# Kernel tuning notes

Hardware: AMD Instinct MI355X
Metric: run time of the kernel (lower is better)

The kernel has to match this reference:

```python
import jax, jax.numpy as jnp
import numpy as np

N_AGENTS = 8
N_HEADS = 4
HYP = 128   # hypernet_embed
EMB = 32    # mixing_embed_dim


def _hypernet(entities, entity_mask, fc1_w, fc1_b, attn_w, out_w, out_b, fc2_w, fc2_b):
    # entities: [B, ne, ed]; entity_mask: [B, ne] (1 = masked/inactive)
    B, ne, _ = entities.shape
    hd = HYP // N_HEADS
    x1 = jax.nn.relu(entities @ fc1_w + fc1_b)                      # [B, ne, HYP]
    am = entity_mask[:, :N_AGENTS].astype(x1.dtype)                 # [B, na]
    em = entity_mask.astype(x1.dtype)                               # [B, ne]
    # attn_mask[b,i,j] = 1 - (1-am[i])*(1-em[j]): mask if agent i OR entity j inactive
    pre_mask = 1.0 - (1.0 - am)[:, :, None] * (1.0 - em)[:, None, :]  # [B, na, ne]
    # EntityAttentionLayer: agents are the queries, all entities are keys/values
    qkv = x1 @ attn_w                                               # [B, ne, 3*HYP] (no bias)
    q, k, v = jnp.split(qkv, 3, axis=-1)
    q = q[:, :N_AGENTS].reshape(B, N_AGENTS, N_HEADS, hd)
    k = k.reshape(B, ne, N_HEADS, hd)
    v = v.reshape(B, ne, N_HEADS, hd)
    scale = jnp.asarray(np.sqrt(hd), x1.dtype)
    logits = jnp.einsum('bqhd,bkhd->bhqk', q, k) / scale            # [B, H, na, ne]
    m = pre_mask[:, None, :, :]
    # masked softmax; fully-masked rows (torch: -inf -> NaN -> 0) become 0 via *(1-m)
    w = jax.nn.softmax(jnp.where(m > 0, -1e30, logits), axis=-1) * (1.0 - m)
    attn = jnp.einsum('bhqk,bkhd->bqhd', w, v).reshape(B, N_AGENTS, HYP)
    attn = attn @ out_w + out_b                                     # [B, na, HYP]
    keep = (1.0 - am)[:, :, None]                                   # zero masked agents (post_mask)
    attn = attn * keep
    x3 = (attn @ fc2_w + fc2_b) * keep                              # [B, na, EMB]
    return x3


def reference(agent_qs, entities, entity_mask, fc1_w, fc1_b, attn_w, out_w, out_b, fc2_w, fc2_b):
    bs, T, ne, ed = entities.shape
    B = bs * T
    ents = entities.reshape(B, ne, ed)
    emask = entity_mask.reshape(B, ne)
    qs = agent_qs.reshape(B, N_AGENTS)
    # 4 hypernets: 0=hyper_w_1 (matrix), 1=hyper_w_final (vector), 2=hyper_b_1 (vector), 3=V (scalar)
    outs = [_hypernet(ents, emask, fc1_w[i], fc1_b[i], attn_w[i], out_w[i],
                      out_b[i], fc2_w[i], fc2_b[i]) for i in range(4)]
    w1 = jax.nn.softmax(outs[0], axis=-1)                           # [B, na, EMB]
    b1 = outs[2].mean(axis=1)                                       # [B, EMB]
    hidden = jax.nn.elu(jnp.einsum('ba,bae->be', qs, w1) + b1)      # [B, EMB]
    w_final = jax.nn.softmax(outs[1].mean(axis=1), axis=-1)         # [B, EMB]
    v = outs[3].mean(axis=(1, 2))                                   # [B]
    y = jnp.sum(hidden * w_final, axis=-1) + v                      # [B]
    return y.reshape(bs, T, 1)


def setup_inputs() -> dict:
    key = jax.random.key(0)
    ks = jax.random.split(key, 10)
    bs, T, ne, ed = 128, 64, 16, 64
    s = 0.05
    return {
        'agent_qs': jax.random.normal(ks[0], (bs, T, N_AGENTS), jnp.float32),
        'entities': jax.random.normal(ks[1], (bs, T, ne, ed), jnp.float32),
        'entity_mask': jax.random.randint(ks[2], (bs, T, ne), 0, 2, jnp.int32),
        'fc1_w': jax.random.normal(ks[3], (4, ed, HYP), jnp.float32) * s,
        'fc1_b': jax.random.normal(ks[4], (4, HYP), jnp.float32) * s,
        'attn_w': jax.random.normal(ks[5], (4, HYP, 3 * HYP), jnp.float32) * s,
        'out_w': jax.random.normal(ks[6], (4, HYP, HYP), jnp.float32) * s,
        'out_b': jax.random.normal(ks[7], (4, HYP), jnp.float32) * s,
        'fc2_w': jax.random.normal(ks[8], (4, HYP, EMB), jnp.float32) * s,
        'fc2_b': jax.random.normal(ks[9], (4, EMB), jnp.float32) * s,
    }
```

## Files before the change

kernel.cpp:

```cpp
#include <hip/hip_runtime.h>
#include <math.h>

#define NAG 8
#define NE  16
#define ED  64
#define HYPD 128
#define QKVW 384
#define SB 4

#define X1S 132
#define KS  132
#define QS  132

#define OFF_X1    0
#define OFF_SLOG  0
#define OFF_ATTN  8448
#define OFF_K     16896
#define OFF_ATTN2 16896
#define OFF_Q     33792
#define OFF_OUT0  42240
#define OFF_MEANS 44288
#define OFF_EM    45824
#define LDS_BYTES 46080

typedef __attribute__((ext_vector_type(8))) short bf16x8;
typedef __attribute__((ext_vector_type(4))) short bf16x4;
typedef __attribute__((ext_vector_type(4))) float f32x4;

__device__ __forceinline__ short f2bf(float f) {
    union { float f; unsigned u; } c; c.f = f;
    unsigned r = (c.u + 0x7FFFu + ((c.u >> 16) & 1u)) >> 16;
    return (short)r;
}
__device__ __forceinline__ float bf2f(short s) {
    union { unsigned u; float f; } c; c.u = ((unsigned)(unsigned short)s) << 16; return c.f;
}
__device__ __forceinline__ bf16x8 ld_frag(const short* p) {
    bf16x4 lo = *(const bf16x4*)p;
    bf16x4 hi = *(const bf16x4*)(p + 16);
    return __builtin_shufflevector(lo, hi, 0, 1, 2, 3, 4, 5, 6, 7);
}

__global__ void pack_weights(const float* __restrict__ fc1_w,
                             const float* __restrict__ attn_w,
                             const float* __restrict__ out_w,
                             const float* __restrict__ fc2_w,
                             short* __restrict__ ws) {
    int gid = blockIdx.x * 256 + threadIdx.x;
    if (gid >= 608 * 64) return;
    int slot = gid >> 6, l = gid & 63;
    const float* src; int N, nt, kt;
    if (slot < 64) {
        int h = slot >> 4, f = slot & 15;
        nt = f >> 1; kt = f & 1; N = HYPD; src = fc1_w + h * ED * HYPD;
    } else if (slot < 448) {
        int s2 = slot - 64; int h = s2 / 96, f = s2 % 96;
        nt = f >> 2; kt = f & 3; N = QKVW; src = attn_w + h * HYPD * QKVW;
    } else if (slot < 576) {
        int s2 = slot - 448; int h = s2 >> 5, f = s2 & 31;
        nt = f >> 2; kt = f & 3; N = HYPD; src = out_w + h * HYPD * HYPD;
    } else {
        int s2 = slot - 576; int h = s2 >> 3, f = s2 & 7;
        nt = f >> 2; kt = f & 3; N = 32; src = fc2_w + h * HYPD * 32;
    }
    int rg = l >> 4, lc = l & 15;
    bf16x8 fr;
    #pragma unroll
    for (int j = 0; j < 8; ++j) {
        int k = kt * 32 + 4 * rg + (j & 3) + 16 * (j >> 2);
        fr[j] = f2bf(src[k * N + nt * 16 + lc]);
    }
    ((bf16x8*)ws)[slot * 64 + l] = fr;
}

__global__ __launch_bounds__(256, 2) void flexq_mfma(
    const float* __restrict__ agent_qs,
    const float* __restrict__ entities,
    const int*   __restrict__ entity_mask,
    const float* __restrict__ fc1_b,
    const float* __restrict__ out_b,
    const float* __restrict__ fc2_b,
    const short* __restrict__ wfrag,
    float* __restrict__ out, int B)
{
    __shared__ __align__(16) char smem[LDS_BYTES];
    short* x1    = (short*)(smem + OFF_X1);
    float* slog  = (float*)(smem + OFF_SLOG);
    short* attn  = (short*)(smem + OFF_ATTN);
    short* k     = (short*)(smem + OFF_K);
    short* attn2 = (short*)(smem + OFF_ATTN2);
    short* q     = (short*)(smem + OFF_Q);
    short* out0  = (short*)(smem + OFF_OUT0);
    float* means = (float*)(smem + OFF_MEANS);
    float* em    = (float*)(smem + OFF_EM);

    const int tid = threadIdx.x;
    const int l = tid & 63, w = tid >> 6;
    const int rg = l >> 4, lc = l & 15;
    const int b4 = blockIdx.x * SB;
    const bf16x8* WF = (const bf16x8*)wfrag;

    if (tid < 64)
        em[tid] = (entity_mask[(size_t)b4 * NE + tid] != 0) ? 1.0f : 0.0f;

    bf16x8 aent[2][4];
    #pragma unroll
    for (int kt = 0; kt < 2; ++kt)
        #pragma unroll
        for (int mt = 0; mt < 4; ++mt) {
            const float* ap = entities + ((size_t)(b4 + mt) * NE + lc) * ED + kt * 32 + rg * 4;
            float4 lo = *(const float4*)ap;
            float4 hi = *(const float4*)(ap + 16);
            bf16x8 af;
            af[0]=f2bf(lo.x); af[1]=f2bf(lo.y); af[2]=f2bf(lo.z); af[3]=f2bf(lo.w);
            af[4]=f2bf(hi.x); af[5]=f2bf(hi.y); af[6]=f2bf(hi.z); af[7]=f2bf(hi.w);
            aent[kt][mt] = af;
        }
    __syncthreads();

    for (int i = 0; i < 4; ++i) {
        {
            f32x4 acc[4][2];
            #pragma unroll
            for (int mt = 0; mt < 4; ++mt) {
                acc[mt][0] = (f32x4){0.f,0.f,0.f,0.f};
                acc[mt][1] = (f32x4){0.f,0.f,0.f,0.f};
            }
            #pragma unroll
            for (int kt = 0; kt < 2; ++kt) {
                bf16x8 b0 = WF[(i*16 + (2*w+0)*2 + kt)*64 + l];
                bf16x8 b1 = WF[(i*16 + (2*w+1)*2 + kt)*64 + l];
                #pragma unroll
                for (int mt = 0; mt < 4; ++mt) {
                    acc[mt][0] = __builtin_amdgcn_mfma_f32_16x16x32_bf16(aent[kt][mt], b0, acc[mt][0], 0,0,0);
                    acc[mt][1] = __builtin_amdgcn_mfma_f32_16x16x32_bf16(aent[kt][mt], b1, acc[mt][1], 0,0,0);
                }
            }
            float bias0 = fc1_b[i*HYPD + 32*w + lc];
            float bias1 = fc1_b[i*HYPD + 32*w + 16 + lc];
            #pragma unroll
            for (int mt = 0; mt < 4; ++mt)
                #pragma unroll
                for (int r = 0; r < 4; ++r) {
                    int row = 16*mt + 4*rg + r;
                    x1[row*X1S + 32*w + lc]      = f2bf(fmaxf(acc[mt][0][r] + bias0, 0.f));
                    x1[row*X1S + 32*w + 16 + lc] = f2bf(fmaxf(acc[mt][1][r] + bias1, 0.f));
                }
        }
        __syncthreads();

        f32x4 accv[4][2];
        {
            f32x4 acc[4][3];
            #pragma unroll
            for (int mt = 0; mt < 4; ++mt)
                #pragma unroll
                for (int n = 0; n < 3; ++n) acc[mt][n] = (f32x4){0.f,0.f,0.f,0.f};
            #pragma unroll
            for (int kt = 0; kt < 4; ++kt) {
                bf16x8 b0 = WF[(64 + i*96 + (w +  0)*4 + kt)*64 + l];
                bf16x8 b1 = WF[(64 + i*96 + (w +  4)*4 + kt)*64 + l];
                bf16x8 b2 = WF[(64 + i*96 + (w +  8)*4 + kt)*64 + l];
                #pragma unroll
                for (int mt = 0; mt < 4; ++mt) {
                    bf16x8 a = ld_frag(x1 + (16*mt + lc)*X1S + kt*32 + rg*4);
                    acc[mt][0] = __builtin_amdgcn_mfma_f32_16x16x32_bf16(a, b0, acc[mt][0], 0,0,0);
                    acc[mt][1] = __builtin_amdgcn_mfma_f32_16x16x32_bf16(a, b1, acc[mt][1], 0,0,0);
                    acc[mt][2] = __builtin_amdgcn_mfma_f32_16x16x32_bf16(a, b2, acc[mt][2], 0,0,0);
                }
            }
            #pragma unroll
            for (int mt = 0; mt < 4; ++mt)
                #pragma unroll
                for (int r = 0; r < 4; ++r) {
                    if (rg < 2) {
                        q[(mt*NAG + 4*rg + r)*QS + (w+0)*16 + lc] = f2bf(acc[mt][0][r]);
                        q[(mt*NAG + 4*rg + r)*QS + (w+4)*16 + lc] = f2bf(acc[mt][1][r]);
                    }
                    k[(16*mt + 4*rg + r)*KS + w*16 + lc] = f2bf(acc[mt][2][r]);
                }
        }
        {
            f32x4 acck[4];
            #pragma unroll
            for (int mt = 0; mt < 4; ++mt) {
                acck[mt] = (f32x4){0.f,0.f,0.f,0.f};
                accv[mt][0] = (f32x4){0.f,0.f,0.f,0.f};
                accv[mt][1] = (f32x4){0.f,0.f,0.f,0.f};
            }
            #pragma unroll
            for (int kt = 0; kt < 4; ++kt) {
                bf16x8 b0 = WF[(64 + i*96 + (w + 12)*4 + kt)*64 + l];
                bf16x8 b1 = WF[(64 + i*96 + (w + 16)*4 + kt)*64 + l];
                bf16x8 b2 = WF[(64 + i*96 + (w + 20)*4 + kt)*64 + l];
                #pragma unroll
                for (int mt = 0; mt < 4; ++mt) {
                    bf16x8 a = ld_frag(x1 + (16*mt + lc)*X1S + kt*32 + rg*4);
                    acck[mt]    = __builtin_amdgcn_mfma_f32_16x16x32_bf16(a, b0, acck[mt], 0,0,0);
                    accv[mt][0] = __builtin_amdgcn_mfma_f32_16x16x32_bf16(a, b1, accv[mt][0], 0,0,0);
                    accv[mt][1] = __builtin_amdgcn_mfma_f32_16x16x32_bf16(a, b2, accv[mt][1], 0,0,0);
                }
            }
            #pragma unroll
            for (int mt = 0; mt < 4; ++mt)
                #pragma unroll
                for (int r = 0; r < 4; ++r)
                    k[(16*mt + 4*rg + r)*KS + (w+4)*16 + lc] = f2bf(acck[mt][r]);
        }
        __syncthreads();

        {
            #pragma unroll
            for (int pp = 0; pp < 4; ++pp) {
                int p = 4*w + pp, s = p >> 2, h = p & 3;
                bf16x8 a  = ld_frag(q + (s*NAG + (lc & 7))*QS + h*32 + rg*4);
                bf16x8 bb = ld_frag(k + (s*NE  + lc)*KS       + h*32 + rg*4);
                f32x4 acc = (f32x4){0.f,0.f,0.f,0.f};
                acc = __builtin_amdgcn_mfma_f32_16x16x32_bf16(a, bb, acc, 0,0,0);
                if (rg < 2) {
                    #pragma unroll
                    for (int r = 0; r < 4; ++r)
                        slog[((s*4 + h)*NAG + 4*rg + r)*16 + lc] = acc[r] * 0.17677669529663687f;
                }
            }
        }
        __syncthreads();

        if (tid < 128) {
            int s = tid >> 5, h = (tid >> 3) & 3, qi = tid & 7;
            float am = em[s*NE + qi];
            float* rowp = slog + ((s*4 + h)*NAG + qi)*16;
            float mx = -3.0e38f; bool any = false;
            #pragma unroll
            for (int kk = 0; kk < NE; ++kk)
                if (em[s*NE + kk] == 0.f) { any = true; mx = fmaxf(mx, rowp[kk]); }
            if (am != 0.f || !any) {
                #pragma unroll
                for (int kk = 0; kk < NE; ++kk) rowp[kk] = 0.f;
            } else {
                float eb[NE]; float sum = 0.f;
                #pragma unroll
                for (int kk = 0; kk < NE; ++kk) {
                    float e = (em[s*NE + kk] == 0.f) ? __expf(rowp[kk] - mx) : 0.f;
                    eb[kk] = e; sum += e;
                }
                float inv = 1.f / sum;
                #pragma unroll
                for (int kk = 0; kk < NE; ++kk) rowp[kk] = eb[kk] * inv;
            }
        }
        __syncthreads();

        {
            #pragma unroll
            for (int vt = 0; vt < 2; ++vt) {
                int c = w + 4*vt;
                int h = c >> 1;
                #pragma unroll
                for (int mt = 0; mt < 4; ++mt) {
                    f32x4 pw = *(const f32x4*)(slog + ((mt*4 + h)*NAG + (lc & 7))*16 + 4*rg);
                    bf16x8 a;
                    a[0]=f2bf(pw[0]); a[1]=f2bf(pw[1]); a[2]=f2bf(pw[2]); a[3]=f2bf(pw[3]);
                    a[4]=0; a[5]=0; a[6]=0; a[7]=0;
                    bf16x8 bb;
                    bb[0]=f2bf(accv[mt][vt][0]); bb[1]=f2bf(accv[mt][vt][1]);
                    bb[2]=f2bf(accv[mt][vt][2]); bb[3]=f2bf(accv[mt][vt][3]);
                    bb[4]=0; bb[5]=0; bb[6]=0; bb[7]=0;
                    f32x4 po = (f32x4){0.f,0.f,0.f,0.f};
                    po = __builtin_amdgcn_mfma_f32_16x16x32_bf16(a, bb, po, 0,0,0);
                    if (rg < 2) {
                        #pragma unroll
                        for (int r = 0; r < 4; ++r)
                            attn[(mt*NAG + 4*rg + r)*X1S + c*16 + lc] = f2bf(po[r]);
                    }
                }
            }
        }
        __syncthreads();

        {
            f32x4 acc[2][2];
            #pragma unroll
            for (int mt = 0; mt < 2; ++mt) {
                acc[mt][0] = (f32x4){0.f,0.f,0.f,0.f};
                acc[mt][1] = (f32x4){0.f,0.f,0.f,0.f};
            }
            #pragma unroll
            for (int kt = 0; kt < 4; ++kt) {
                bf16x8 b0 = WF[(448 + i*32 + (2*w+0)*4 + kt)*64 + l];
                bf16x8 b1 = WF[(448 + i*32 + (2*w+1)*4 + kt)*64 + l];
                #pragma unroll
                for (int mt = 0; mt < 2; ++mt) {
                    bf16x8 a = ld_frag(attn + (16*mt + lc)*X1S + kt*32 + rg*4);
                    acc[mt][0] = __builtin_amdgcn_mfma_f32_16x16x32_bf16(a, b0, acc[mt][0], 0,0,0);
                    acc[mt][1] = __builtin_amdgcn_mfma_f32_16x16x32_bf16(a, b1, acc[mt][1], 0,0,0);
                }
            }
            float bias0 = out_b[i*HYPD + 32*w + lc];
            float bias1 = out_b[i*HYPD + 32*w + 16 + lc];
            #pragma unroll
            for (int mt = 0; mt < 2; ++mt)
                #pragma unroll
                for (int r = 0; r < 4; ++r) {
                    int row = 16*mt + 4*rg + r;
                    float keep = 1.f - em[(row >> 3)*NE + (row & 7)];
                    attn2[row*X1S + 32*w + lc]      = f2bf((acc[mt][0][r] + bias0) * keep);
                    attn2[row*X1S + 32*w + 16 + lc] = f2bf((acc[mt][1][r] + bias1) * keep);
                }
        }
        __syncthreads();

        {
            int mt = w >> 1, nt = w & 1;
            f32x4 acc = (f32x4){0.f,0.f,0.f,0.f};
            #pragma unroll
            for (int kt = 0; kt < 4; ++kt) {
                bf16x8 a = ld_frag(attn2 + (16*mt + lc)*X1S + kt*32 + rg*4);
                bf16x8 bfr = WF[(576 + i*8 + nt*4 + kt)*64 + l];
                acc = __builtin_amdgcn_mfma_f32_16x16x32_bf16(a, bfr, acc, 0,0,0);
            }
            float bias = fc2_b[i*32 + nt*16 + lc];
            float vals[4];
            #pragma unroll
            for (int r = 0; r < 4; ++r) {
                int row = 16*mt + 4*rg + r;
                float keep = 1.f - em[(row >> 3)*NE + (row & 7)];
                vals[r] = (acc[r] + bias) * keep;
            }
            if (i == 0) {
                #pragma unroll
                for (int r = 0; r < 4; ++r)
                    out0[(16*mt + 4*rg + r)*32 + nt*16 + lc] = f2bf(vals[r]);
            } else {
                float ps = vals[0] + vals[1] + vals[2] + vals[3];
                ps += __shfl_xor(ps, 16);
                if ((rg & 1) == 0) {
                    int s = 2*mt + (rg >> 1);
                    means[(i-1)*128 + s*32 + nt*16 + lc] = ps;
                }
            }
        }
        __syncthreads();
    }

    if (l < 32) {
        int s = w, c = l;
        float s1 = means[0*128 + s*32 + c] * 0.125f;
        float b1 = means[1*128 + s*32 + c] * 0.125f;
        float vsum = means[2*128 + s*32 + c];

        float hid = 0.f;
        #pragma unroll
        for (int a = 0; a < NAG; ++a) {
            float x = bf2f(out0[(s*NAG + a)*32 + c]);
            float mx = x;
            #pragma unroll
            for (int m = 16; m >= 1; m >>= 1) mx = fmaxf(mx, __shfl_xor(mx, m, 32));
            float e = __expf(x - mx);
            float sum = e;
            #pragma unroll
            for (int m = 16; m >= 1; m >>= 1) sum += __shfl_xor(sum, m, 32);
            float qsv = agent_qs[(size_t)(b4 + s)*NAG + a];
            hid += qsv * (e / sum);
        }
        hid += b1;
        hid = (hid > 0.f) ? hid : expm1f(hid);

        float mx = s1;
        #pragma unroll
        for (int m = 16; m >= 1; m >>= 1) mx = fmaxf(mx, __shfl_xor(mx, m, 32));
        float e = __expf(s1 - mx);
        float ss = e;
        #pragma unroll
        for (int m = 16; m >= 1; m >>= 1) ss += __shfl_xor(ss, m, 32);
        float wf = e / ss;

        float red = hid * wf + vsum * (1.f / 256.f);
        #pragma unroll
        for (int m = 16; m >= 1; m >>= 1) red += __shfl_xor(red, m, 32);
        if (c == 0) out[b4 + s] = red;
    }
}

#define QKVP 388
#define NTHR 384
__device__ __forceinline__ float4 f4load(const float* p) { return *reinterpret_cast<const float4*>(p); }
__device__ __forceinline__ void f4store(float* p, const float4& v) { *reinterpret_cast<float4*>(p) = v; }
__device__ __forceinline__ void f4fma(float4& a, float s, const float4& w) {
    a.x += s * w.x; a.y += s * w.y; a.z += s * w.z; a.w += s * w.w;
}

__global__ __launch_bounds__(NTHR) void flexq_fp32(
    const float* __restrict__ agent_qs, const float* __restrict__ entities,
    const int* __restrict__ entity_mask, const float* __restrict__ fc1_w,
    const float* __restrict__ fc1_b, const float* __restrict__ attn_w,
    const float* __restrict__ out_w, const float* __restrict__ out_b,
    const float* __restrict__ fc2_w, const float* __restrict__ fc2_b,
    float* __restrict__ out)
{
    const int b = blockIdx.x, tid = threadIdx.x;
    __shared__ float s_ent[NE][ED];
    __shared__ float s_x1t[HYPD][NE];
    __shared__ float s_qkv[NE][QKVP];
    __shared__ float s_w[4][NAG][NE];
    __shared__ float s_attn[NAG][HYPD];
    __shared__ float s_attnout[NAG][HYPD];
    __shared__ float s_outs[4][NAG][32];
    __shared__ float s_mask[NE];
    __shared__ float s_qs[NAG];

    const float* ent = entities + (size_t)b * NE * ED;
    for (int o = tid; o < NE * ED; o += NTHR) s_ent[o >> 6][o & 63] = ent[o];
    if (tid < NE) s_mask[tid] = (entity_mask[(size_t)b * NE + tid] != 0) ? 1.0f : 0.0f;
    if (tid < NAG) s_qs[tid] = agent_qs[(size_t)b * NAG + tid];
    __syncthreads();

    for (int i = 0; i < 4; ++i) {
        {
            const float* W1 = fc1_w + i * ED * HYPD;
            const float* B1 = fc1_b + i * HYPD;
            for (int o4 = tid; o4 < 512; o4 += NTHR) {
                int e = o4 >> 5, j = (o4 & 31) * 4;
                float4 acc = f4load(B1 + j);
                for (int d = 0; d < ED; ++d) { float x = s_ent[e][d]; f4fma(acc, x, f4load(W1 + d * HYPD + j)); }
                s_x1t[j+0][e] = fmaxf(acc.x, 0.f); s_x1t[j+1][e] = fmaxf(acc.y, 0.f);
                s_x1t[j+2][e] = fmaxf(acc.z, 0.f); s_x1t[j+3][e] = fmaxf(acc.w, 0.f);
            }
        }
        __syncthreads();
        {
            const float* W2 = attn_w + i * HYPD * QKVW;
            int j = (tid % 96) * 4, e0 = (tid / 96) * 4;
            float4 a0 = {0,0,0,0}, a1 = {0,0,0,0}, a2 = {0,0,0,0}, a3 = {0,0,0,0};
            for (int d = 0; d < HYPD; ++d) {
                float4 wv = f4load(W2 + d * QKVW + j);
                float4 x = f4load(&s_x1t[d][e0]);
                f4fma(a0, x.x, wv); f4fma(a1, x.y, wv); f4fma(a2, x.z, wv); f4fma(a3, x.w, wv);
            }
            f4store(&s_qkv[e0+0][j], a0); f4store(&s_qkv[e0+1][j], a1);
            f4store(&s_qkv[e0+2][j], a2); f4store(&s_qkv[e0+3][j], a3);
        }
        __syncthreads();
        {
            const float inv_scale = 0.17677669529663687f;
            for (int o = tid; o < 512; o += NTHR) {
                int h = o >> 7, qi = (o >> 4) & 7, kk = o & 15;
                const float* qp = &s_qkv[qi][h * 32];
                const float* kp = &s_qkv[kk][HYPD + h * 32];
                float s = 0.f;
                #pragma unroll
                for (int d4 = 0; d4 < 8; ++d4) {
                    float4 qv = f4load(qp + 4 * d4), kv2 = f4load(kp + 4 * d4);
                    s += qv.x*kv2.x + qv.y*kv2.y + qv.z*kv2.z + qv.w*kv2.w;
                }
                s_w[h][qi][kk] = s * inv_scale;
            }
        }
        __syncthreads();
        if (tid < 32) {
            int h = tid >> 3, qi = tid & 7;
            float am = s_mask[qi];
            float mx = -3.0e38f; bool any = false;
            #pragma unroll
            for (int kk = 0; kk < NE; ++kk)
                if (s_mask[kk] == 0.f) { any = true; mx = fmaxf(mx, s_w[h][qi][kk]); }
            if (am != 0.f || !any) {
                #pragma unroll
                for (int kk = 0; kk < NE; ++kk) s_w[h][qi][kk] = 0.f;
            } else {
                float eb[NE]; float sum = 0.f;
                #pragma unroll
                for (int kk = 0; kk < NE; ++kk) {
                    float e = (s_mask[kk] == 0.f) ? __expf(s_w[h][qi][kk] - mx) : 0.f;
                    eb[kk] = e; sum += e;
                }
                float inv = 1.f / sum;
                #pragma unroll
                for (int kk = 0; kk < NE; ++kk) s_w[h][qi][kk] = eb[kk] * inv;
            }
        }
        __syncthreads();
        if (tid < 256) {
            int qi = tid >> 5, j = (tid & 31) * 4, h = j >> 5, d0 = j & 31;
            float4 acc = {0,0,0,0};
            #pragma unroll
            for (int kk = 0; kk < NE; ++kk) f4fma(acc, s_w[h][qi][kk], f4load(&s_qkv[kk][2*HYPD + h*32 + d0]));
            f4store(&s_attn[qi][j], acc);
        }
        __syncthreads();
        if (tid < 256) {
            const float* W3 = out_w + i * HYPD * HYPD;
            const float* B3 = out_b + i * HYPD;
            int qi = tid >> 5, j = (tid & 31) * 4;
            float4 acc = f4load(B3 + j);
            for (int d = 0; d < HYPD; ++d) f4fma(acc, s_attn[qi][d], f4load(W3 + d * HYPD + j));
            float keep = 1.f - s_mask[qi];
            acc.x *= keep; acc.y *= keep; acc.z *= keep; acc.w *= keep;
            f4store(&s_attnout[qi][j], acc);
        }
        __syncthreads();
        if (tid < 64) {
            const float* W4 = fc2_w + i * HYPD * 32;
            const float* B4 = fc2_b + i * 32;
            int qi = tid >> 3, c = (tid & 7) * 4;
            float4 acc = f4load(B4 + c);
            for (int d = 0; d < HYPD; ++d) f4fma(acc, s_attnout[qi][d], f4load(W4 + d * 32 + c));
            float keep = 1.f - s_mask[qi];
            acc.x *= keep; acc.y *= keep; acc.z *= keep; acc.w *= keep;
            f4store(&s_outs[i][qi][c], acc);
        }
        __syncthreads();
    }

    if (tid < 32) {
        const int c = tid;
        float b1 = 0.f, s1 = 0.f, vs = 0.f;
        #pragma unroll
        for (int qi = 0; qi < NAG; ++qi) {
            b1 += s_outs[2][qi][c]; s1 += s_outs[1][qi][c]; vs += s_outs[3][qi][c];
        }
        b1 *= 0.125f; s1 *= 0.125f;
        float hid = 0.f;
        #pragma unroll
        for (int a = 0; a < NAG; ++a) {
            float x = s_outs[0][a][c];
            float mx = x;
            #pragma unroll
            for (int m = 16; m >= 1; m >>= 1) mx = fmaxf(mx, __shfl_xor(mx, m, 32));
            float e = __expf(x - mx);
            float sm = e;
            #pragma unroll
            for (int m = 16; m >= 1; m >>= 1) sm += __shfl_xor(sm, m, 32);
            hid += s_qs[a] * (e / sm);
        }
        hid += b1;
        hid = (hid > 0.f) ? hid : expm1f(hid);
        float mx = s1;
        #pragma unroll
        for (int m = 16; m >= 1; m >>= 1) mx = fmaxf(mx, __shfl_xor(mx, m, 32));
        float e = __expf(s1 - mx);
        float ssum = e;
        #pragma unroll
        for (int m = 16; m >= 1; m >>= 1) ssum += __shfl_xor(ssum, m, 32);
        float wf = e / ssum;
        float red = hid * wf + vs * (1.f / 256.f);
        #pragma unroll
        for (int m = 16; m >= 1; m >>= 1) red += __shfl_xor(red, m, 32);
        if (tid == 0) out[b] = red;
    }
}

extern "C" void kernel_launch(void* const* d_in, const int* in_sizes, int n_in,
                              void* d_out, int out_size, void* d_ws, size_t ws_size,
                              hipStream_t stream) {
    const float* agent_qs    = (const float*)d_in[0];
    const float* entities    = (const float*)d_in[1];
    const int*   entity_mask = (const int*)  d_in[2];
    const float* fc1_w       = (const float*)d_in[3];
    const float* fc1_b       = (const float*)d_in[4];
    const float* attn_w      = (const float*)d_in[5];
    const float* out_w       = (const float*)d_in[6];
    const float* out_b       = (const float*)d_in[7];
    const float* fc2_w       = (const float*)d_in[8];
    const float* fc2_b       = (const float*)d_in[9];
    float* out = (float*)d_out;

    const int B = in_sizes[0] / NAG;

    if (ws_size >= (size_t)(608 * 1024) && (B % SB) == 0) {
        pack_weights<<<152, 256, 0, stream>>>(fc1_w, attn_w, out_w, fc2_w, (short*)d_ws);
        flexq_mfma<<<B / SB, 256, 0, stream>>>(agent_qs, entities, entity_mask,
                                               fc1_b, out_b, fc2_b,
                                               (const short*)d_ws, out, B);
    } else {
        flexq_fp32<<<B, NTHR, 0, stream>>>(agent_qs, entities, entity_mask,
                                           fc1_w, fc1_b, attn_w, out_w, out_b,
                                           fc2_w, fc2_b, out);
    }
}
```

Baseline: 186.6 us.

## Shrink MFMA blocks to two samples with 128 threads and remap wave work

Each block now handles two batch samples with two waves instead of four samples with four waves, which halves LDS use and doubles the grid size. Each wave takes on more N-tiles per GEMM stage so the tile loops and the attention, out-projection and fc2 work are redistributed. The intent is more resident blocks per CU and finer-grained scheduling. In exchange, each block reuses each weight fragment across fewer rows, so global and L2 traffic for the packed weights roughly doubles.

```diff
diff --git a/kernel.cpp b/kernel.cpp
--- a/kernel.cpp
+++ b/kernel.cpp
@@ -6,7 +6,7 @@
 #define ED  64
 #define HYPD 128
 #define QKVW 384
-#define SB 4
+#define SB 2
 
 #define X1S 132
 #define KS  132
@@ -14,14 +14,14 @@
 
 #define OFF_X1    0
 #define OFF_SLOG  0
-#define OFF_ATTN  8448
-#define OFF_K     16896
-#define OFF_ATTN2 16896
-#define OFF_Q     33792
-#define OFF_OUT0  42240
-#define OFF_MEANS 44288
-#define OFF_EM    45824
-#define LDS_BYTES 46080
+#define OFF_ATTN  4224
+#define OFF_K     8448
+#define OFF_ATTN2 8448
+#define OFF_Q     16896
+#define OFF_OUT0  21120
+#define OFF_MEANS 22144
+#define OFF_EM    22912
+#define LDS_BYTES 23040
 
 typedef __attribute__((ext_vector_type(8))) short bf16x8;
 typedef __attribute__((ext_vector_type(4))) short bf16x4;
@@ -73,7 +73,7 @@
     ((bf16x8*)ws)[slot * 64 + l] = fr;
 }
 
-__global__ __launch_bounds__(256, 2) void flexq_mfma(
+__global__ __launch_bounds__(128, 2) void flexq_mfma(
     const float* __restrict__ agent_qs,
     const float* __restrict__ entities,
     const int*   __restrict__ entity_mask,
@@ -97,18 +97,18 @@
     const int tid = threadIdx.x;
     const int l = tid & 63, w = tid >> 6;
     const int rg = l >> 4, lc = l & 15;
-    const int b4 = blockIdx.x * SB;
+    const int b2 = blockIdx.x * SB;
     const bf16x8* WF = (const bf16x8*)wfrag;
 
-    if (tid < 64)
-        em[tid] = (entity_mask[(size_t)b4 * NE + tid] != 0) ? 1.0f : 0.0f;
-
-    bf16x8 aent[2][4];
+    if (tid < 32)
+        em[tid] = (entity_mask[(size_t)b2 * NE + tid] != 0) ? 1.0f : 0.0f;
+
+    bf16x8 aent[2][2];
     #pragma unroll
     for (int kt = 0; kt < 2; ++kt)
         #pragma unroll
-        for (int mt = 0; mt < 4; ++mt) {
-            const float* ap = entities + ((size_t)(b4 + mt) * NE + lc) * ED + kt * 32 + rg * 4;
+        for (int mt = 0; mt < 2; ++mt) {
+            const float* ap = entities + ((size_t)(b2 + mt) * NE + lc) * ED + kt * 32 + rg * 4;
             float4 lo = *(const float4*)ap;
             float4 hi = *(const float4*)(ap + 16);
             bf16x8 af;
@@ -120,113 +120,129 @@
 
     for (int i = 0; i < 4; ++i) {
         {
-            f32x4 acc[4][2];
-            #pragma unroll
-            for (int mt = 0; mt < 4; ++mt) {
-                acc[mt][0] = (f32x4){0.f,0.f,0.f,0.f};
-                acc[mt][1] = (f32x4){0.f,0.f,0.f,0.f};
-            }
+            f32x4 acc[2][4];
+            #pragma unroll
+            for (int mt = 0; mt < 2; ++mt)
+                #pragma unroll
+                for (int n = 0; n < 4; ++n) acc[mt][n] = (f32x4){0.f,0.f,0.f,0.f};
             #pragma unroll
             for (int kt = 0; kt < 2; ++kt) {
-                bf16x8 b0 = WF[(i*16 + (2*w+0)*2 + kt)*64 + l];
-                bf16x8 b1 = WF[(i*16 + (2*w+1)*2 + kt)*64 + l];
-                #pragma unroll
-                for (int mt = 0; mt < 4; ++mt) {
-                    acc[mt][0] = __builtin_amdgcn_mfma_f32_16x16x32_bf16(aent[kt][mt], b0, acc[mt][0], 0,0,0);
-                    acc[mt][1] = __builtin_amdgcn_mfma_f32_16x16x32_bf16(aent[kt][mt], b1, acc[mt][1], 0,0,0);
-                }
-            }
-            float bias0 = fc1_b[i*HYPD + 32*w + lc];
-            float bias1 = fc1_b[i*HYPD + 32*w + 16 + lc];
-            #pragma unroll
-            for (int mt = 0; mt < 4; ++mt)
-                #pragma unroll
-                for (int r = 0; r < 4; ++r) {
-                    int row = 16*mt + 4*rg + r;
-                    x1[row*X1S + 32*w + lc]      = f2bf(fmaxf(acc[mt][0][r] + bias0, 0.f));
-                    x1[row*X1S + 32*w + 16 + lc] = f2bf(fmaxf(acc[mt][1][r] + bias1, 0.f));
-                }
-        }
-        __syncthreads();
-
-        f32x4 accv[4][2];
-        {
-            f32x4 acc[4][3];
-            #pragma unroll
-            for (int mt = 0; mt < 4; ++mt)
-                #pragma unroll
-                for (int n = 0; n < 3; ++n) acc[mt][n] = (f32x4){0.f,0.f,0.f,0.f};
+                bf16x8 bn[4];
+                #pragma unroll
+                for (int n = 0; n < 4; ++n) bn[n] = WF[(i*16 + (4*w+n)*2 + kt)*64 + l];
+                #pragma unroll
+                for (int mt = 0; mt < 2; ++mt)
+                    #pragma unroll
+                    for (int n = 0; n < 4; ++n)
+                        acc[mt][n] = __builtin_amdgcn_mfma_f32_16x16x32_bf16(aent[kt][mt], bn[n], acc[mt][n], 0,0,0);
+            }
+            #pragma unroll
+            for (int n = 0; n < 4; ++n) {
+                float bias = fc1_b[i*HYPD + (4*w+n)*16 + lc];
+                #pragma unroll
+                for (int mt = 0; mt < 2; ++mt)
+                    #pragma unroll
+                    for (int r = 0; r < 4; ++r)
+                        x1[(16*mt + 4*rg + r)*X1S + (4*w+n)*16 + lc] = f2bf(fmaxf(acc[mt][n][r] + bias, 0.f));
+            }
+        }
+        __syncthreads();
+
+        f32x4 accv[2][4];
+        {
+            f32x4 acc[2][4];
+            #pragma unroll
+            for (int mt = 0; mt < 2; ++mt)
+                #pragma unroll
+                for (int j = 0; j < 4; ++j) acc[mt][j] = (f32x4){0.f,0.f,0.f,0.f};
             #pragma unroll
             for (int kt = 0; kt < 4; ++kt) {
-                bf16x8 b0 = WF[(64 + i*96 + (w +  0)*4 + kt)*64 + l];
-                bf16x8 b1 = WF[(64 + i*96 + (w +  4)*4 + kt)*64 + l];
-                bf16x8 b2 = WF[(64 + i*96 + (w +  8)*4 + kt)*64 + l];
-                #pragma unroll
-                for (int mt = 0; mt < 4; ++mt) {
+                bf16x8 bj[4];
+                #pragma unroll
+                for (int j = 0; j < 4; ++j) bj[j] = WF[(64 + i*96 + (w + 2*j)*4 + kt)*64 + l];
+                #pragma unroll
+                for (int mt = 0; mt < 2; ++mt) {
                     bf16x8 a = ld_frag(x1 + (16*mt + lc)*X1S + kt*32 + rg*4);
-                    acc[mt][0] = __builtin_amdgcn_mfma_f32_16x16x32_bf16(a, b0, acc[mt][0], 0,0,0);
-                    acc[mt][1] = __builtin_amdgcn_mfma_f32_16x16x32_bf16(a, b1, acc[mt][1], 0,0,0);
-                    acc[mt][2] = __builtin_amdgcn_mfma_f32_16x16x32_bf16(a, b2, acc[mt][2], 0,0,0);
-                }
-            }
-            #pragma unroll
-            for (int mt = 0; mt < 4; ++mt)
-                #pragma unroll
-                for (int r = 0; r < 4; ++r) {
-                    if (rg < 2) {
-                        q[(mt*NAG + 4*rg + r)*QS + (w+0)*16 + lc] = f2bf(acc[mt][0][r]);
-                        q[(mt*NAG + 4*rg + r)*QS + (w+4)*16 + lc] = f2bf(acc[mt][1][r]);
-                    }
-                    k[(16*mt + 4*rg + r)*KS + w*16 + lc] = f2bf(acc[mt][2][r]);
-                }
-        }
-        {
-            f32x4 acck[4];
-            #pragma unroll
-            for (int mt = 0; mt < 4; ++mt) {
-                acck[mt] = (f32x4){0.f,0.f,0.f,0.f};
-                accv[mt][0] = (f32x4){0.f,0.f,0.f,0.f};
-                accv[mt][1] = (f32x4){0.f,0.f,0.f,0.f};
-            }
+                    #pragma unroll
+                    for (int j = 0; j < 4; ++j)
+                        acc[mt][j] = __builtin_amdgcn_mfma_f32_16x16x32_bf16(a, bj[j], acc[mt][j], 0,0,0);
+                }
+            }
+            if (rg < 2) {
+                #pragma unroll
+                for (int j = 0; j < 4; ++j)
+                    #pragma unroll
+                    for (int mt = 0; mt < 2; ++mt)
+                        #pragma unroll
+                        for (int r = 0; r < 4; ++r)
+                            q[(mt*NAG + 4*rg + r)*QS + (w + 2*j)*16 + lc] = f2bf(acc[mt][j][r]);
+            }
+        }
+        {
+            f32x4 acc[2][4];
+            #pragma unroll
+            for (int mt = 0; mt < 2; ++mt)
+                #pragma unroll
+                for (int j = 0; j < 4; ++j) acc[mt][j] = (f32x4){0.f,0.f,0.f,0.f};
             #pragma unroll
             for (int kt = 0; kt < 4; ++kt) {
-                bf16x8 b0 = WF[(64 + i*96 + (w + 12)*4 + kt)*64 + l];
-                bf16x8 b1 = WF[(64 + i*96 + (w + 16)*4 + kt)*64 + l];
-                bf16x8 b2 = WF[(64 + i*96 + (w + 20)*4 + kt)*64 + l];
-                #pragma unroll
-                for (int mt = 0; mt < 4; ++mt) {
+                bf16x8 bj[4];
+                #pragma unroll
+                for (int j = 0; j < 4; ++j) bj[j] = WF[(64 + i*96 + (8 + w + 2*j)*4 + kt)*64 + l];
+                #pragma unroll
+                for (int mt = 0; mt < 2; ++mt) {
                     bf16x8 a = ld_frag(x1 + (16*mt + lc)*X1S + kt*32 + rg*4);
-                    acck[mt]    = __builtin_amdgcn_mfma_f32_16x16x32_bf16(a, b0, acck[mt], 0,0,0);
-                    accv[mt][0] = __builtin_amdgcn_mfma_f32_16x16x32_bf16(a, b1, accv[mt][0], 0,0,0);
-                    accv[mt][1] = __builtin_amdgcn_mfma_f32_16x16x32_bf16(a, b2, accv[mt][1], 0,0,0);
-                }
-            }
-            #pragma unroll
-            for (int mt = 0; mt < 4; ++mt)
-                #pragma unroll
-                for (int r = 0; r < 4; ++r)
-                    k[(16*mt + 4*rg + r)*KS + (w+4)*16 + lc] = f2bf(acck[mt][r]);
-        }
-        __syncthreads();
-
-        {
-            #pragma unroll
-            for (int pp = 0; pp < 4; ++pp) {
-                int p = 4*w + pp, s = p >> 2, h = p & 3;
-                bf16x8 a  = ld_frag(q + (s*NAG + (lc & 7))*QS + h*32 + rg*4);
-                bf16x8 bb = ld_frag(k + (s*NE  + lc)*KS       + h*32 + rg*4);
+                    #pragma unroll
+                    for (int j = 0; j < 4; ++j)
+                        acc[mt][j] = __builtin_amdgcn_mfma_f32_16x16x32_bf16(a, bj[j], acc[mt][j], 0,0,0);
+                }
+            }
+            #pragma unroll
+            for (int j = 0; j < 4; ++j)
+                #pragma unroll
+                for (int mt = 0; mt < 2; ++mt)
+                    #pragma unroll
+                    for (int r = 0; r < 4; ++r)
+                        k[(16*mt + 4*rg + r)*KS + (w + 2*j)*16 + lc] = f2bf(acc[mt][j][r]);
+        }
+        {
+            #pragma unroll
+            for (int mt = 0; mt < 2; ++mt)
+                #pragma unroll
+                for (int j = 0; j < 4; ++j) accv[mt][j] = (f32x4){0.f,0.f,0.f,0.f};
+            #pragma unroll
+            for (int kt = 0; kt < 4; ++kt) {
+                bf16x8 bj[4];
+                #pragma unroll
+                for (int j = 0; j < 4; ++j) bj[j] = WF[(64 + i*96 + (16 + w + 2*j)*4 + kt)*64 + l];
+                #pragma unroll
+                for (int mt = 0; mt < 2; ++mt) {
+                    bf16x8 a = ld_frag(x1 + (16*mt + lc)*X1S + kt*32 + rg*4);
+                    #pragma unroll
+                    for (int j = 0; j < 4; ++j)
+                        accv[mt][j] = __builtin_amdgcn_mfma_f32_16x16x32_bf16(a, bj[j], accv[mt][j], 0,0,0);
+                }
+            }
+        }
+        __syncthreads();
+
+        {
+            #pragma unroll
+            for (int h = 0; h < 4; ++h) {
+                bf16x8 a  = ld_frag(q + (w*NAG + (lc & 7))*QS + h*32 + rg*4);
+                bf16x8 bb = ld_frag(k + (w*NE  + lc)*KS       + h*32 + rg*4);
                 f32x4 acc = (f32x4){0.f,0.f,0.f,0.f};
                 acc = __builtin_amdgcn_mfma_f32_16x16x32_bf16(a, bb, acc, 0,0,0);
                 if (rg < 2) {
                     #pragma unroll
                     for (int r = 0; r < 4; ++r)
-                        slog[((s*4 + h)*NAG + 4*rg + r)*16 + lc] = acc[r] * 0.17677669529663687f;
-                }
-            }
-        }
-        __syncthreads();
-
-        if (tid < 128) {
+                        slog[((w*4 + h)*NAG + 4*rg + r)*16 + lc] = acc[r] * 0.17677669529663687f;
+                }
+            }
+        }
+        __syncthreads();
+
+        if (tid < 64) {
             int s = tid >> 5, h = (tid >> 3) & 3, qi = tid & 7;
             float am = em[s*NE + qi];
             float* rowp = slog + ((s*4 + h)*NAG + qi)*16;
@@ -253,11 +269,11 @@
 
         {
             #pragma unroll
-            for (int vt = 0; vt < 2; ++vt) {
-                int c = w + 4*vt;
+            for (int vt = 0; vt < 4; ++vt) {
+                int c = w + 2*vt;
                 int h = c >> 1;
                 #pragma unroll
-                for (int mt = 0; mt < 4; ++mt) {
+                for (int mt = 0; mt < 2; ++mt) {
                     f32x4 pw = *(const f32x4*)(slog + ((mt*4 + h)*NAG + (lc & 7))*16 + 4*rg);
                     bf16x8 a;
                     a[0]=f2bf(pw[0]); a[1]=f2bf(pw[1]); a[2]=f2bf(pw[2]); a[3]=f2bf(pw[3]);
@@ -279,64 +295,58 @@
         __syncthreads();
 
         {
-            f32x4 acc[2][2];
-            #pragma unroll
-            for (int mt = 0; mt < 2; ++mt) {
-                acc[mt][0] = (f32x4){0.f,0.f,0.f,0.f};
-                acc[mt][1] = (f32x4){0.f,0.f,0.f,0.f};
-            }
+            f32x4 acc[4];
+            #pragma unroll
+            for (int n = 0; n < 4; ++n) acc[n] = (f32x4){0.f,0.f,0.f,0.f};
             #pragma unroll
             for (int kt = 0; kt < 4; ++kt) {
-                bf16x8 b0 = WF[(448 + i*32 + (2*w+0)*4 + kt)*64 + l];
-                bf16x8 b1 = WF[(448 + i*32 + (2*w+1)*4 + kt)*64 + l];
-                #pragma unroll
-                for (int mt = 0; mt < 2; ++mt) {
-                    bf16x8 a = ld_frag(attn + (16*mt + lc)*X1S + kt*32 + rg*4);
-                    acc[mt][0] = __builtin_amdgcn_mfma_f32_16x16x32_bf16(a, b0, acc[mt][0], 0,0,0);
-                    acc[mt][1] = __builtin_amdgcn_mfma_f32_16x16x32_bf16(a, b1, acc[mt][1], 0,0,0);
-                }
-            }
-            float bias0 = out_b[i*HYPD + 32*w + lc];
-            float bias1 = out_b[i*HYPD + 32*w + 16 + lc];
-            #pragma unroll
-            for (int mt = 0; mt < 2; ++mt)
+                bf16x8 bn[4];
+                #pragma unroll
+                for (int n = 0; n < 4; ++n) bn[n] = WF[(448 + i*32 + (4*w+n)*4 + kt)*64 + l];
+                bf16x8 a = ld_frag(attn + lc*X1S + kt*32 + rg*4);
+                #pragma unroll
+                for (int n = 0; n < 4; ++n)
+                    acc[n] = __builtin_amdgcn_mfma_f32_16x16x32_bf16(a, bn[n], acc[n], 0,0,0);
+            }
+            #pragma unroll
+            for (int n = 0; n < 4; ++n) {
+                float bias = out_b[i*HYPD + (4*w+n)*16 + lc];
                 #pragma unroll
                 for (int r = 0; r < 4; ++r) {
-                    int row = 16*mt + 4*rg + r;
+                    int row = 4*rg + r;
                     float keep = 1.f - em[(row >> 3)*NE + (row & 7)];
-                    attn2[row*X1S + 32*w + lc]      = f2bf((acc[mt][0][r] + bias0) * keep);
-                    attn2[row*X1S + 32*w + 16 + lc] = f2bf((acc[mt][1][r] + bias1) * keep);
-                }
-        }
-        __syncthreads();
-
-        {
-            int mt = w >> 1, nt = w & 1;
+                    attn2[row*X1S + (4*w+n)*16 + lc] = f2bf((acc[n][r] + bias) * keep);
+                }
+            }
+        }
+        __syncthreads();
+
+        {
             f32x4 acc = (f32x4){0.f,0.f,0.f,0.f};
             #pragma unroll
             for (int kt = 0; kt < 4; ++kt) {
-                bf16x8 a = ld_frag(attn2 + (16*mt + lc)*X1S + kt*32 + rg*4);
-                bf16x8 bfr = WF[(576 + i*8 + nt*4 + kt)*64 + l];
+                bf16x8 a = ld_frag(attn2 + lc*X1S + kt*32 + rg*4);
+                bf16x8 bfr = WF[(576 + i*8 + w*4 + kt)*64 + l];
                 acc = __builtin_amdgcn_mfma_f32_16x16x32_bf16(a, bfr, acc, 0,0,0);
             }
-            float bias = fc2_b[i*32 + nt*16 + lc];
+            float bias = fc2_b[i*32 + w*16 + lc];
             float vals[4];
             #pragma unroll
             for (int r = 0; r < 4; ++r) {
-                int row = 16*mt + 4*rg + r;
+                int row = 4*rg + r;
                 float keep = 1.f - em[(row >> 3)*NE + (row & 7)];
                 vals[r] = (acc[r] + bias) * keep;
             }
             if (i == 0) {
                 #pragma unroll
                 for (int r = 0; r < 4; ++r)
-                    out0[(16*mt + 4*rg + r)*32 + nt*16 + lc] = f2bf(vals[r]);
+                    out0[(4*rg + r)*32 + w*16 + lc] = f2bf(vals[r]);
             } else {
                 float ps = vals[0] + vals[1] + vals[2] + vals[3];
                 ps += __shfl_xor(ps, 16);
                 if ((rg & 1) == 0) {
-                    int s = 2*mt + (rg >> 1);
-                    means[(i-1)*128 + s*32 + nt*16 + lc] = ps;
+                    int s = rg >> 1;
+                    means[(i-1)*64 + s*32 + w*16 + lc] = ps;
                 }
             }
         }
@@ -345,9 +355,9 @@
 
     if (l < 32) {
         int s = w, c = l;
-        float s1 = means[0*128 + s*32 + c] * 0.125f;
-        float b1 = means[1*128 + s*32 + c] * 0.125f;
-        float vsum = means[2*128 + s*32 + c];
+        float s1 = means[0*64 + s*32 + c] * 0.125f;
+        float b1 = means[1*64 + s*32 + c] * 0.125f;
+        float vsum = means[2*64 + s*32 + c];
 
         float hid = 0.f;
         #pragma unroll
@@ -360,7 +370,7 @@
             float sum = e;
             #pragma unroll
             for (int m = 16; m >= 1; m >>= 1) sum += __shfl_xor(sum, m, 32);
-            float qsv = agent_qs[(size_t)(b4 + s)*NAG + a];
+            float qsv = agent_qs[(size_t)(b2 + s)*NAG + a];
             hid += qsv * (e / sum);
         }
         hid += b1;
@@ -378,7 +388,7 @@
         float red = hid * wf + vsum * (1.f / 256.f);
         #pragma unroll
         for (int m = 16; m >= 1; m >>= 1) red += __shfl_xor(red, m, 32);
-        if (c == 0) out[b4 + s] = red;
+        if (c == 0) out[b2 + s] = red;
     }
 }
 
@@ -569,7 +579,7 @@
 
     if (ws_size >= (size_t)(608 * 1024) && (B % SB) == 0) {
         pack_weights<<<152, 256, 0, stream>>>(fc1_w, attn_w, out_w, fc2_w, (short*)d_ws);
-        flexq_mfma<<<B / SB, 256, 0, stream>>>(agent_qs, entities, entity_mask,
+        flexq_mfma<<<B / SB, 128, 0, stream>>>(agent_qs, entities, entity_mask,
                                                fc1_b, out_b, fc2_b,
                                                (const short*)d_ws, out, B);
     } else {
```

Result: slower. 199.0 us (+6.6%).
